# Kernel tuning notes

Hardware: AMD Instinct MI355X
Metric: run time of the kernel (lower is better)

Reference implementation:

```python
import jax, jax.numpy as jnp
import numpy as np

N_NODES = 100000
N_EDGES = 1600000
N_DATE = 5000  # last N_DATE nodes are date nodes [0,0,1]
D_IN = 128
D_H = 128
N_CLASSES = 16
MLP_HID = 8


def setup_inputs() -> dict:
    key = jax.random.key(0)
    ks = jax.random.split(key, 12)
    feature = jax.random.normal(ks[0], (N_NODES, D_IN), dtype=jnp.float32)
    edge_weight = jax.random.uniform(ks[1], (N_EDGES,), dtype=jnp.float32)
    src = jax.random.randint(ks[2], (N_EDGES,), 0, N_NODES, dtype=jnp.int32)
    dst = jax.random.randint(ks[3], (N_EDGES,), 0, N_NODES, dtype=jnp.int32)
    # node_type one-hot: regular nodes [1,0,0], last N_DATE nodes are date nodes [0,0,1]
    nt = np.zeros((N_NODES, 3), dtype=np.int32)
    nt[: N_NODES - N_DATE, 0] = 1
    nt[N_NODES - N_DATE :, 2] = 1
    node_type = jnp.asarray(nt)
    # GraphConv weights (xavier uniform) + zero bias, DGL convention: h @ W, W:[in,out]
    def xavier(k, fan_in, fan_out):
        lim = float(np.sqrt(6.0 / (fan_in + fan_out)))
        return jax.random.uniform(k, (fan_in, fan_out), jnp.float32, -lim, lim)
    W0 = xavier(ks[4], D_IN, D_H)
    b0 = jnp.zeros((D_H,), jnp.float32)
    W1 = xavier(ks[5], D_H, D_H)
    b1 = jnp.zeros((D_H,), jnp.float32)
    mlp_w1 = xavier(ks[6], D_H, MLP_HID)
    mlp_b1 = jnp.zeros((MLP_HID,), jnp.float32)
    mlp_w2 = xavier(ks[7], MLP_HID, N_CLASSES)
    mlp_b2 = jnp.zeros((N_CLASSES,), jnp.float32)
    return {
        "feature": feature, "edge_weight": edge_weight, "src": src, "dst": dst,
        "node_type": node_type, "W0": W0, "b0": b0, "W1": W1, "b1": b1,
        "mlp_w1": mlp_w1, "mlp_b1": mlp_b1, "mlp_w2": mlp_w2, "mlp_b2": mlp_b2,
    }


def reference(feature, edge_weight, src, dst, node_type,
              W0, b0, W1, b1, mlp_w1, mlp_b1, mlp_w2, mlp_b2):
    n = feature.shape[0]
    ones_e = jnp.ones_like(edge_weight)
    # unweighted degrees (DGL norm='both'), clamped to >= 1
    deg_out = jnp.clip(jax.ops.segment_sum(ones_e, src, num_segments=n), 1.0)
    deg_in = jnp.clip(jax.ops.segment_sum(ones_e, dst, num_segments=n), 1.0)
    norm_src = deg_out ** -0.5  # [N]
    norm_dst = deg_in ** -0.5   # [N]

    def graph_conv(h, W, b):
        hn = h * norm_src[:, None]                      # D_out^{-1/2} src scaling
        msg = hn[src] * edge_weight[:, None]            # [E, d] edge-weighted gather
        agg = jax.ops.segment_sum(msg, dst, num_segments=n)  # scatter-add
        return (agg * norm_dst[:, None]) @ W + b        # D_in^{-1/2}, then linear

    h = jax.nn.relu(graph_conv(feature, W0, b0))
    h = jax.nn.relu(graph_conv(h, W1, b1))

    # sum-pool over date nodes ([0,0,1]) == tail slice in original layout
    date_mask = ((node_type[:, 0] == 0) & (node_type[:, 1] == 0) & (node_type[:, 2] == 1)).astype(h.dtype)
    cnt = date_mask.sum()
    pooled = (h * date_mask[:, None]).sum(axis=0) / cnt  # [d_h]

    hid = jax.nn.relu(pooled @ mlp_w1 + mlp_b1)
    return hid @ mlp_w2 + mlp_b2  # [num_classes]
```

## Files before the change

### kernel.cpp

```cpp
#include <hip/hip_runtime.h>
#include <hip/hip_fp16.h>
#include <stdint.h>

#define D 128
#define GT 16
#define SLOTS 48
#define EPB 4096
#define PTB 1024
#define CAPE 5120
#define MAXB 400
#define MAXDATE 8192
#define WPN 16384

typedef _Float16 f16x8 __attribute__((ext_vector_type(8)));
typedef float    f32x4 __attribute__((ext_vector_type(4)));

__global__ __launch_bounds__(PTB) void partition_kernel(
    const int* __restrict__ src, const int* __restrict__ dst, const float* __restrict__ ew,
    int* __restrict__ cursorA, int* __restrict__ cursorB,
    int2* __restrict__ ebuf, int* __restrict__ sbuf, int E, int nbk) {
    __shared__ int histA[MAXB], histB[MAXB], baseA[MAXB], baseB[MAXB];
    int tid = threadIdx.x;
    for (int i = tid; i < nbk; i += PTB) { histA[i] = 0; histB[i] = 0; }
    __syncthreads();
    int e0 = blockIdx.x * EPB;
    int dcache[EPB / PTB], scache[EPB / PTB];
    float wcache[EPB / PTB];
    #pragma unroll
    for (int i = 0; i < EPB / PTB; ++i) {
        int e = e0 + i * PTB + tid;
        bool ok = e < E;
        dcache[i] = ok ? dst[e] : -1;
        scache[i] = ok ? src[e] : 0;
        wcache[i] = ok ? ew[e] : 0.f;
        if (ok) {
            atomicAdd(&histA[dcache[i] >> 8], 1);
            atomicAdd(&histB[scache[i] >> 8], 1);
        }
    }
    __syncthreads();
    for (int i = tid; i < nbk; i += PTB) {
        baseA[i] = atomicAdd(&cursorA[i], histA[i]);
        baseB[i] = atomicAdd(&cursorB[i], histB[i]);
        histA[i] = 0; histB[i] = 0;
    }
    __syncthreads();
    #pragma unroll
    for (int i = 0; i < EPB / PTB; ++i) {
        if (dcache[i] >= 0) {
            int d = dcache[i], s = scache[i];
            int bA = d >> 8;
            int pA = baseA[bA] + atomicAdd(&histA[bA], 1);
            if (pA < CAPE) ebuf[(size_t)bA * CAPE + pA] =
                make_int2(s | ((d & 255) << 17), __float_as_int(wcache[i]));
            int bB = s >> 8;
            int pB = baseB[bB] + atomicAdd(&histB[bB], 1);
            if (pB < CAPE) sbuf[(size_t)bB * CAPE + pB] = s;
        }
    }
}

__global__ __launch_bounds__(256) void build_count_kernel(
    const int2* __restrict__ ebuf, const int* __restrict__ cursorA,
    const int* __restrict__ sbuf, const int* __restrict__ cursorB,
    int2* __restrict__ ell, int* __restrict__ deg_in, int* __restrict__ deg_out,
    int n, int nbk) {
    __shared__ int lcur[256];
    int tid = threadIdx.x;
    lcur[tid] = 0;
    __syncthreads();
    if (blockIdx.x < (unsigned)nbk) {
        int b = blockIdx.x;
        int cntE = min(cursorA[b], CAPE);
        const int2* buf = ebuf + (size_t)b * CAPE;
        for (int i = tid; i < cntE; i += 256) {
            int2 r = buf[i];
            int s = r.x & 0x1FFFF;
            int dlow = (r.x >> 17) & 255;
            int slot = atomicAdd(&lcur[dlow], 1);
            int node = (b << 8) + dlow;
            if (slot < SLOTS) ell[(size_t)node * SLOTS + slot] = make_int2(s, r.y);
        }
        __syncthreads();
        int v = (b << 8) + tid;
        if (v < n) deg_in[v] = lcur[tid];
    } else {
        int b = blockIdx.x - nbk;
        int cntS = min(cursorB[b], CAPE);
        const int* buf = sbuf + (size_t)b * CAPE;
        for (int i = tid; i < cntS; i += 256) {
            atomicAdd(&lcur[buf[i] & 255], 1);
        }
        __syncthreads();
        int v = (b << 8) + tid;
        if (v < n) deg_out[v] = lcur[tid];
    }
}

__global__ void norm_flag_kernel(const int* __restrict__ deg_out, const int* __restrict__ deg_in,
                                 const int* __restrict__ node_type,
                                 float* __restrict__ norm_src, float* __restrict__ norm_dst,
                                 int* __restrict__ list, int* __restrict__ cnt, int n) {
    int v = blockIdx.x * blockDim.x + threadIdx.x;
    if (v < n) {
        float d_o = (float)max(deg_out[v], 1);
        float d_i = (float)max(deg_in[v], 1);
        norm_src[v] = 1.0f / sqrtf(d_o);
        norm_dst[v] = 1.0f / sqrtf(d_i);
        int t0 = node_type[v * 3 + 0];
        int t1 = node_type[v * 3 + 1];
        int t2 = node_type[v * 3 + 2];
        if (t0 == 0 && t1 == 0 && t2 == 1) {
            int idx = atomicAdd(cnt, 1);
            list[idx] = v;
        }
    }
}

__global__ __launch_bounds__(256) void wpack_kernel(const float* __restrict__ W,
                                                    _Float16* __restrict__ wp) {
    int base = blockIdx.x * 256 + threadIdx.x;
    for (int idx = base; idx < WPN; idx += gridDim.x * 256) {
        int j = idx & 7;
        int l = (idx >> 3) & 63;
        int c = (idx >> 9) & 7;
        int k0b = idx >> 12;
        int q = l >> 4, r = l & 15;
        float w = W[(k0b * 32 + q * 8 + j) * 128 + c * 16 + r];
        _Float16 hi = (_Float16)w;
        wp[idx] = hi;
        wp[idx + WPN] = (_Float16)(w - (float)hi);
    }
}

__global__ __launch_bounds__(256) void gemm_mfma_kernel(
    const float* __restrict__ X, const float* __restrict__ ns,
    const _Float16* __restrict__ wp, _Float16* __restrict__ P, int n) {
    int lane = threadIdx.x & 63;
    int wib  = threadIdx.x >> 6;
    int q = lane >> 4, r = lane & 15;
    int row0 = blockIdx.x * 128 + wib * 32;
    if (row0 >= n) return;
    int ra = min(row0 + r,      n - 1);
    int rb = min(row0 + 16 + r, n - 1);
    float sa = ns[ra];
    float sb = ns[rb];

    f32x4 acc[2][8];
    #pragma unroll
    for (int t = 0; t < 2; ++t)
        #pragma unroll
        for (int c = 0; c < 8; ++c)
            acc[t][c] = (f32x4){0.f, 0.f, 0.f, 0.f};

    for (int k0 = 0; k0 < 128; k0 += 32) {
        float4 xa0 = *(const float4*)&X[(size_t)ra * 128 + k0 + q * 8];
        float4 xa1 = *(const float4*)&X[(size_t)ra * 128 + k0 + q * 8 + 4];
        float4 xb0 = *(const float4*)&X[(size_t)rb * 128 + k0 + q * 8];
        float4 xb1 = *(const float4*)&X[(size_t)rb * 128 + k0 + q * 8 + 4];
        f16x8 a0, a1;
        a0[0] = (_Float16)(xa0.x * sa); a0[1] = (_Float16)(xa0.y * sa);
        a0[2] = (_Float16)(xa0.z * sa); a0[3] = (_Float16)(xa0.w * sa);
        a0[4] = (_Float16)(xa1.x * sa); a0[5] = (_Float16)(xa1.y * sa);
        a0[6] = (_Float16)(xa1.z * sa); a0[7] = (_Float16)(xa1.w * sa);
        a1[0] = (_Float16)(xb0.x * sb); a1[1] = (_Float16)(xb0.y * sb);
        a1[2] = (_Float16)(xb0.z * sb); a1[3] = (_Float16)(xb0.w * sb);
        a1[4] = (_Float16)(xb1.x * sb); a1[5] = (_Float16)(xb1.y * sb);
        a1[6] = (_Float16)(xb1.z * sb); a1[7] = (_Float16)(xb1.w * sb);
        const _Float16* wb = wp + (size_t)(k0 >> 5) * 4096 + lane * 8;
        #pragma unroll
        for (int c = 0; c < 8; ++c) {
            f16x8 bh = *(const f16x8*)&wb[c * 512];
            f16x8 bl = *(const f16x8*)&wb[c * 512 + WPN];
            acc[0][c] = __builtin_amdgcn_mfma_f32_16x16x32_f16(a0, bh, acc[0][c], 0, 0, 0);
            acc[0][c] = __builtin_amdgcn_mfma_f32_16x16x32_f16(a0, bl, acc[0][c], 0, 0, 0);
            acc[1][c] = __builtin_amdgcn_mfma_f32_16x16x32_f16(a1, bh, acc[1][c], 0, 0, 0);
            acc[1][c] = __builtin_amdgcn_mfma_f32_16x16x32_f16(a1, bl, acc[1][c], 0, 0, 0);
        }
    }

    #pragma unroll
    for (int t = 0; t < 2; ++t) {
        #pragma unroll
        for (int j = 0; j < 4; ++j) {
            int row = row0 + t * 16 + q * 4 + j;
            if (row < n) {
                #pragma unroll
                for (int c = 0; c < 8; ++c) {
                    P[(size_t)row * 128 + c * 16 + r] = (_Float16)acc[t][c][j];
                }
            }
        }
    }
}

__global__ __launch_bounds__(256) void gather1_kernel(
    const __half* __restrict__ P, const int* __restrict__ deg_in,
    const int2* __restrict__ ell, const float* __restrict__ norm_src,
    const float* __restrict__ norm_dst, const float* __restrict__ bias,
    __half* __restrict__ h1, int n) {
    int wave = (blockIdx.x * 256 + threadIdx.x) >> 6;
    int lane = threadIdx.x & 63;
    if (wave >= n) return;
    int v = __builtin_amdgcn_readfirstlane(wave);
    int m = min(deg_in[v], SLOTS);
    const int2* row = ell + (size_t)v * SLOTS;
    int half = lane >> 5;
    int l32  = lane & 31;
    float4 acc = make_float4(0.f, 0.f, 0.f, 0.f);
    for (int e = 0; e < m; e += 4) {
        int4 qa = *(const int4*)&row[e];
        int4 qb = *(const int4*)&row[e + 2];
        int2 p0 = half ? make_int2(qa.z, qa.w) : make_int2(qa.x, qa.y);
        int2 p1 = half ? make_int2(qb.z, qb.w) : make_int2(qb.x, qb.y);
        bool v0 = (e + half) < m;
        bool v1 = (e + 2 + half) < m;
        int s0 = v0 ? p0.x : 0;
        int s1 = v1 ? p1.x : 0;
        float2 raw0 = ((const float2*)P)[(size_t)s0 * 32 + l32];
        float2 raw1 = ((const float2*)P)[(size_t)s1 * 32 + l32];
        float w0 = v0 ? __int_as_float(p0.y) : 0.f;
        float w1 = v1 ? __int_as_float(p1.y) : 0.f;
        float2 a01 = __half22float2(*(const __half2*)&raw0.x);
        float2 a23 = __half22float2(*(const __half2*)&raw0.y);
        float2 b01 = __half22float2(*(const __half2*)&raw1.x);
        float2 b23 = __half22float2(*(const __half2*)&raw1.y);
        acc.x = fmaf(w0, a01.x, acc.x); acc.x = fmaf(w1, b01.x, acc.x);
        acc.y = fmaf(w0, a01.y, acc.y); acc.y = fmaf(w1, b01.y, acc.y);
        acc.z = fmaf(w0, a23.x, acc.z); acc.z = fmaf(w1, b23.x, acc.z);
        acc.w = fmaf(w0, a23.y, acc.w); acc.w = fmaf(w1, b23.y, acc.w);
    }
    acc.x += __shfl_xor(acc.x, 32);
    acc.y += __shfl_xor(acc.y, 32);
    acc.z += __shfl_xor(acc.z, 32);
    acc.w += __shfl_xor(acc.w, 32);
    if (half == 0) {
        float nd = norm_dst[v];
        float ns = norm_src[v];
        float4 b4 = ((const float4*)bias)[l32];
        float ra = fmaxf(fmaf(acc.x, nd, b4.x), 0.f) * ns;
        float rb = fmaxf(fmaf(acc.y, nd, b4.y), 0.f) * ns;
        float rc = fmaxf(fmaf(acc.z, nd, b4.z), 0.f) * ns;
        float rd = fmaxf(fmaf(acc.w, nd, b4.w), 0.f) * ns;
        __half2 h0 = __floats2half2_rn(ra, rb);
        __half2 h1v = __floats2half2_rn(rc, rd);
        uint2 u;
        u.x = *(unsigned int*)&h0;
        u.y = *(unsigned int*)&h1v;
        ((uint2*)h1)[(size_t)v * 32 + l32] = u;
    }
}

__global__ __launch_bounds__(256) void gather2_list_kernel(
    const __half* __restrict__ h, const int* __restrict__ deg_in,
    const int2* __restrict__ ell, const float* __restrict__ norm_dst,
    const int* __restrict__ list, const int* __restrict__ cnt,
    float* __restrict__ out) {
    int wave = (blockIdx.x * 256 + threadIdx.x) >> 6;
    int lane = threadIdx.x & 63;
    if (wave >= min(*cnt, MAXDATE)) return;
    int v = __builtin_amdgcn_readfirstlane(list[wave]);
    int m = min(deg_in[v], SLOTS);
    const int2* row = ell + (size_t)v * SLOTS;
    int half = lane >> 5;
    int l32  = lane & 31;
    float4 acc = make_float4(0.f, 0.f, 0.f, 0.f);
    for (int e = 0; e < m; e += 4) {
        int4 qa = *(const int4*)&row[e];
        int4 qb = *(const int4*)&row[e + 2];
        int2 p0 = half ? make_int2(qa.z, qa.w) : make_int2(qa.x, qa.y);
        int2 p1 = half ? make_int2(qb.z, qb.w) : make_int2(qb.x, qb.y);
        bool v0 = (e + half) < m;
        bool v1 = (e + 2 + half) < m;
        int s0 = v0 ? p0.x : 0;
        int s1 = v1 ? p1.x : 0;
        float2 raw0 = ((const float2*)h)[(size_t)s0 * 32 + l32];
        float2 raw1 = ((const float2*)h)[(size_t)s1 * 32 + l32];
        float w0 = v0 ? __int_as_float(p0.y) : 0.f;
        float w1 = v1 ? __int_as_float(p1.y) : 0.f;
        float2 a01 = __half22float2(*(const __half2*)&raw0.x);
        float2 a23 = __half22float2(*(const __half2*)&raw0.y);
        float2 b01 = __half22float2(*(const __half2*)&raw1.x);
        float2 b23 = __half22float2(*(const __half2*)&raw1.y);
        acc.x = fmaf(w0, a01.x, acc.x); acc.x = fmaf(w1, b01.x, acc.x);
        acc.y = fmaf(w0, a01.y, acc.y); acc.y = fmaf(w1, b01.y, acc.y);
        acc.z = fmaf(w0, a23.x, acc.z); acc.z = fmaf(w1, b23.x, acc.z);
        acc.w = fmaf(w0, a23.y, acc.w); acc.w = fmaf(w1, b23.y, acc.w);
    }
    acc.x += __shfl_xor(acc.x, 32);
    acc.y += __shfl_xor(acc.y, 32);
    acc.z += __shfl_xor(acc.z, 32);
    acc.w += __shfl_xor(acc.w, 32);
    if (half == 0) {
        float nd = norm_dst[v];
        ((float4*)(out + (size_t)wave * D))[l32] =
            make_float4(acc.x * nd, acc.y * nd, acc.z * nd, acc.w * nd);
    }
}

__global__ __launch_bounds__(256) void gemm_pool_kernel(
    const float* __restrict__ X, const float* __restrict__ W,
    const float* __restrict__ bias, const int* __restrict__ cnt,
    float* __restrict__ pooled) {
    __shared__ float rows[4][GT * D];
    int lane = threadIdx.x & 63;
    int wib  = threadIdx.x >> 6;
    int tile = blockIdx.x * 4 + wib;
    int t0 = tile * GT;
    int m = min(*cnt, MAXDATE);
    if (t0 >= m) return;

    float* rw = rows[wib];
    const float2* X2 = (const float2*)X;
    #pragma unroll
    for (int t = 0; t < GT; ++t) {
        int i = t0 + t;
        float2 r = (i < m) ? X2[(size_t)i * 64 + lane] : make_float2(0.f, 0.f);
        *(float2*)&rw[t * D + 2 * lane] = r;
    }
    __builtin_amdgcn_wave_barrier();

    float2 bb = ((const float2*)bias)[lane];
    float2 acc[GT];
    #pragma unroll
    for (int t = 0; t < GT; ++t) acc[t] = make_float2(0.f, 0.f);

    const float2* W2 = (const float2*)W;
    for (int k = 0; k < D; k += 4) {
        float2 w0 = W2[(k + 0) * 64 + lane];
        float2 w1 = W2[(k + 1) * 64 + lane];
        float2 w2 = W2[(k + 2) * 64 + lane];
        float2 w3 = W2[(k + 3) * 64 + lane];
        #pragma unroll
        for (int t = 0; t < GT; ++t) {
            float4 r = *(const float4*)&rw[t * D + k];
            acc[t].x = fmaf(r.x, w0.x, acc[t].x); acc[t].y = fmaf(r.x, w0.y, acc[t].y);
            acc[t].x = fmaf(r.y, w1.x, acc[t].x); acc[t].y = fmaf(r.y, w1.y, acc[t].y);
            acc[t].x = fmaf(r.z, w2.x, acc[t].x); acc[t].y = fmaf(r.z, w2.y, acc[t].y);
            acc[t].x = fmaf(r.w, w3.x, acc[t].x); acc[t].y = fmaf(r.w, w3.y, acc[t].y);
        }
    }

    float psx = 0.f, psy = 0.f;
    #pragma unroll
    for (int t = 0; t < GT; ++t) {
        if (t0 + t < m) {
            psx += fmaxf(acc[t].x + bb.x, 0.f);
            psy += fmaxf(acc[t].y + bb.y, 0.f);
        }
    }
    atomicAdd(&pooled[2 * lane + 0], psx);
    atomicAdd(&pooled[2 * lane + 1], psy);
}

__global__ void mlp_kernel(const float* __restrict__ pooled, const int* __restrict__ cnt,
                           const float* __restrict__ w1, const float* __restrict__ b1,
                           const float* __restrict__ w2, const float* __restrict__ b2,
                           float* __restrict__ out) {
    __shared__ float hid[8];
    int t = threadIdx.x;
    float inv = 1.0f / (float)(*cnt);
    if (t < 8) {
        float a = b1[t];
        for (int k = 0; k < 128; ++k) a = fmaf(pooled[k] * inv, w1[k * 8 + t], a);
        hid[t] = fmaxf(a, 0.f);
    }
    __syncthreads();
    if (t < 16) {
        float a = b2[t];
        for (int j = 0; j < 8; ++j) a = fmaf(hid[j], w2[j * 16 + t], a);
        out[t] = a;
    }
}

extern "C" void kernel_launch(void* const* d_in, const int* in_sizes, int n_in,
                              void* d_out, int out_size, void* d_ws, size_t ws_size,
                              hipStream_t stream) {
    const float* feature   = (const float*)d_in[0];
    const float* ew        = (const float*)d_in[1];
    const int*   src       = (const int*)d_in[2];
    const int*   dst       = (const int*)d_in[3];
    const int*   node_type = (const int*)d_in[4];
    const float* W0        = (const float*)d_in[5];
    const float* b0        = (const float*)d_in[6];
    const float* W1        = (const float*)d_in[7];
    const float* b1        = (const float*)d_in[8];
    const float* mw1       = (const float*)d_in[9];
    const float* mb1       = (const float*)d_in[10];
    const float* mw2       = (const float*)d_in[11];
    const float* mb2       = (const float*)d_in[12];
    float* out = (float*)d_out;

    const int n = in_sizes[0] / D;
    const int E = in_sizes[1];
    const int NBK = (n + 255) >> 8;

    char* ws = (char*)d_ws;
    size_t off = 0;
    auto alloc = [&](size_t bytes) -> void* {
        void* p = ws + off;
        off = (off + bytes + 255) & ~(size_t)255;
        return p;
    };
    int*      cursorAB = (int*)alloc(2 * MAXB * 4);
    int*      deg_in   = (int*)alloc((size_t)n * 4);
    int*      deg_out  = (int*)alloc((size_t)n * 4);
    float*    norm_src = (float*)alloc((size_t)n * 4);
    float*    norm_dst = (float*)alloc((size_t)n * 4);
    int*      list     = (int*)alloc((size_t)n * 4);
    int2*     ell      = (int2*)alloc(((size_t)n * SLOTS + 8) * 8);
    int2*     ebuf     = (int2*)alloc((size_t)NBK * CAPE * 8);
    int*      sbuf     = (int*)alloc((size_t)NBK * CAPE * 4);
    _Float16* P16      = (_Float16*)alloc((size_t)n * D * 2);
    __half*   h1       = (__half*)alloc((size_t)n * D * 2);
    _Float16* wp       = (_Float16*)alloc(2 * WPN * 2);
    float*    pooled   = (float*)alloc(D * 4);
    int*      cnt      = (int*)alloc(256);
    float*    agg      = (float*)sbuf;

    int* cursorA = cursorAB;
    int* cursorB = cursorAB + MAXB;

    hipMemsetAsync(cursorAB, 0, 2 * MAXB * 4, stream);
    hipMemsetAsync(pooled,   0, D * 4 + 256, stream);

    const int TB = 256;
    int pblk = (E + EPB - 1) / EPB;
    int nblk = (n + TB - 1) / TB;

    wpack_kernel<<<16, TB, 0, stream>>>(W0, wp);
    partition_kernel<<<pblk, PTB, 0, stream>>>(src, dst, ew, cursorA, cursorB, ebuf, sbuf, E, NBK);
    build_count_kernel<<<2 * NBK, TB, 0, stream>>>(ebuf, cursorA, sbuf, cursorB,
                                                   ell, deg_in, deg_out, n, NBK);
    norm_flag_kernel<<<nblk, TB, 0, stream>>>(deg_out, deg_in, node_type,
                                              norm_src, norm_dst, list, cnt, n);

    gemm_mfma_kernel<<<(n + 127) / 128, TB, 0, stream>>>(feature, norm_src, wp, P16, n);

    gather1_kernel<<<(n * 64 + TB - 1) / TB, TB, 0, stream>>>(
        (const __half*)P16, deg_in, ell, norm_src, norm_dst, b0, h1, n);

    gather2_list_kernel<<<(MAXDATE * 64) / TB, TB, 0, stream>>>(
        h1, deg_in, ell, norm_dst, list, cnt, agg);
    gemm_pool_kernel<<<((MAXDATE + GT - 1) / GT + 3) / 4, TB, 0, stream>>>(agg, W1, b1, cnt, pooled);

    mlp_kernel<<<1, 64, 0, stream>>>(pooled, cnt, mw1, mb1, mw2, mb2, out);
}
```

Baseline: 328.6 us.

## Store layer-1 projection in FP8 and fold memsets into weight pack kernel

The layer-1 GEMM output is quantized to FP8 e4m3 instead of fp16, and the edge gather reads 4 bytes per lane and decodes each byte to float. This halves the bytes fetched per gathered neighbor row in the dominant gather kernel. Buffer zeroing for cursors, pooled sums and the date counter moves into the weight-packing kernel, removing two memset launches. FP8 storage reduces precision of the intermediate, risking tolerance failures, and the scalar byte decoding adds ALU work.

```diff
diff --git a/kernel.cpp b/kernel.cpp
--- a/kernel.cpp
+++ b/kernel.cpp
@@ -1,5 +1,6 @@
 #include <hip/hip_runtime.h>
 #include <hip/hip_fp16.h>
+#include <hip/hip_fp8.h>
 #include <stdint.h>
 
 #define D 128
@@ -14,6 +15,12 @@
 
 typedef _Float16 f16x8 __attribute__((ext_vector_type(8)));
 typedef float    f32x4 __attribute__((ext_vector_type(4)));
+
+__device__ __forceinline__ float fp8_dec(unsigned char b) {
+    __hip_fp8_e4m3 t;
+    t.__x = b;
+    return (float)t;
+}
 
 __global__ __launch_bounds__(PTB) void partition_kernel(
     const int* __restrict__ src, const int* __restrict__ dst, const float* __restrict__ ew,
@@ -118,8 +125,17 @@
 }
 
 __global__ __launch_bounds__(256) void wpack_kernel(const float* __restrict__ W,
-                                                    _Float16* __restrict__ wp) {
-    int base = blockIdx.x * 256 + threadIdx.x;
+                                                    _Float16* __restrict__ wp,
+                                                    int* __restrict__ cursorAB,
+                                                    float* __restrict__ pooled,
+                                                    int* __restrict__ cnt) {
+    int tid = threadIdx.x;
+    if (blockIdx.x == 0) {
+        for (int i = tid; i < 2 * MAXB; i += 256) cursorAB[i] = 0;
+        if (tid < D) pooled[tid] = 0.f;
+        if (tid == 0) *cnt = 0;
+    }
+    int base = blockIdx.x * 256 + tid;
     for (int idx = base; idx < WPN; idx += gridDim.x * 256) {
         int j = idx & 7;
         int l = (idx >> 3) & 63;
@@ -135,7 +151,7 @@
 
 __global__ __launch_bounds__(256) void gemm_mfma_kernel(
     const float* __restrict__ X, const float* __restrict__ ns,
-    const _Float16* __restrict__ wp, _Float16* __restrict__ P, int n) {
+    const _Float16* __restrict__ wp, unsigned char* __restrict__ P8, int n) {
     int lane = threadIdx.x & 63;
     int wib  = threadIdx.x >> 6;
     int q = lane >> 4, r = lane & 15;
@@ -187,7 +203,8 @@
             if (row < n) {
                 #pragma unroll
                 for (int c = 0; c < 8; ++c) {
-                    P[(size_t)row * 128 + c * 16 + r] = (_Float16)acc[t][c][j];
+                    __hip_fp8_e4m3 qv((float)acc[t][c][j]);
+                    P8[(size_t)row * 128 + c * 16 + r] = qv.__x;
                 }
             }
         }
@@ -195,7 +212,7 @@
 }
 
 __global__ __launch_bounds__(256) void gather1_kernel(
-    const __half* __restrict__ P, const int* __restrict__ deg_in,
+    const unsigned char* __restrict__ P8, const int* __restrict__ deg_in,
     const int2* __restrict__ ell, const float* __restrict__ norm_src,
     const float* __restrict__ norm_dst, const float* __restrict__ bias,
     __half* __restrict__ h1, int n) {
@@ -207,6 +224,7 @@
     const int2* row = ell + (size_t)v * SLOTS;
     int half = lane >> 5;
     int l32  = lane & 31;
+    const unsigned int* P32 = (const unsigned int*)P8;
     float4 acc = make_float4(0.f, 0.f, 0.f, 0.f);
     for (int e = 0; e < m; e += 4) {
         int4 qa = *(const int4*)&row[e];
@@ -217,18 +235,19 @@
         bool v1 = (e + 2 + half) < m;
         int s0 = v0 ? p0.x : 0;
         int s1 = v1 ? p1.x : 0;
-        float2 raw0 = ((const float2*)P)[(size_t)s0 * 32 + l32];
-        float2 raw1 = ((const float2*)P)[(size_t)s1 * 32 + l32];
-        float w0 = v0 ? __int_as_float(p0.y) : 0.f;
+        unsigned int r0 = P32[(size_t)s0 * 32 + l32];
+        unsigned int r1 = P32[(size_t)s1 * 32 + l32];
+        float w0 = v0 ? __int_as_float(p0.y) * __builtin_amdgcn_readfirstlane(0x3f800000 ? 1.f : 1.f) : 0.f;
+        w0 = v0 ? __int_as_float(p0.y) : 0.f;
         float w1 = v1 ? __int_as_float(p1.y) : 0.f;
-        float2 a01 = __half22float2(*(const __half2*)&raw0.x);
-        float2 a23 = __half22float2(*(const __half2*)&raw0.y);
-        float2 b01 = __half22float2(*(const __half2*)&raw1.x);
-        float2 b23 = __half22float2(*(const __half2*)&raw1.y);
-        acc.x = fmaf(w0, a01.x, acc.x); acc.x = fmaf(w1, b01.x, acc.x);
-        acc.y = fmaf(w0, a01.y, acc.y); acc.y = fmaf(w1, b01.y, acc.y);
-        acc.z = fmaf(w0, a23.x, acc.z); acc.z = fmaf(w1, b23.x, acc.z);
-        acc.w = fmaf(w0, a23.y, acc.w); acc.w = fmaf(w1, b23.y, acc.w);
+        acc.x = fmaf(w0, fp8_dec(r0 & 0xff),         acc.x);
+        acc.y = fmaf(w0, fp8_dec((r0 >> 8) & 0xff),  acc.y);
+        acc.z = fmaf(w0, fp8_dec((r0 >> 16) & 0xff), acc.z);
+        acc.w = fmaf(w0, fp8_dec(r0 >> 24),          acc.w);
+        acc.x = fmaf(w1, fp8_dec(r1 & 0xff),         acc.x);
+        acc.y = fmaf(w1, fp8_dec((r1 >> 8) & 0xff),  acc.y);
+        acc.z = fmaf(w1, fp8_dec((r1 >> 16) & 0xff), acc.z);
+        acc.w = fmaf(w1, fp8_dec(r1 >> 24),          acc.w);
     }
     acc.x += __shfl_xor(acc.x, 32);
     acc.y += __shfl_xor(acc.y, 32);
@@ -402,43 +421,40 @@
         off = (off + bytes + 255) & ~(size_t)255;
         return p;
     };
-    int*      cursorAB = (int*)alloc(2 * MAXB * 4);
-    int*      deg_in   = (int*)alloc((size_t)n * 4);
-    int*      deg_out  = (int*)alloc((size_t)n * 4);
-    float*    norm_src = (float*)alloc((size_t)n * 4);
-    float*    norm_dst = (float*)alloc((size_t)n * 4);
-    int*      list     = (int*)alloc((size_t)n * 4);
-    int2*     ell      = (int2*)alloc(((size_t)n * SLOTS + 8) * 8);
-    int2*     ebuf     = (int2*)alloc((size_t)NBK * CAPE * 8);
-    int*      sbuf     = (int*)alloc((size_t)NBK * CAPE * 4);
-    _Float16* P16      = (_Float16*)alloc((size_t)n * D * 2);
-    __half*   h1       = (__half*)alloc((size_t)n * D * 2);
-    _Float16* wp       = (_Float16*)alloc(2 * WPN * 2);
-    float*    pooled   = (float*)alloc(D * 4);
-    int*      cnt      = (int*)alloc(256);
-    float*    agg      = (float*)sbuf;
+    int*           cursorAB = (int*)alloc(2 * MAXB * 4);
+    int*           deg_in   = (int*)alloc((size_t)n * 4);
+    int*           deg_out  = (int*)alloc((size_t)n * 4);
+    float*         norm_src = (float*)alloc((size_t)n * 4);
+    float*         norm_dst = (float*)alloc((size_t)n * 4);
+    int*           list     = (int*)alloc((size_t)n * 4);
+    int2*          ell      = (int2*)alloc(((size_t)n * SLOTS + 8) * 8);
+    int2*          ebuf     = (int2*)alloc((size_t)NBK * CAPE * 8);
+    int*           sbuf     = (int*)alloc((size_t)NBK * CAPE * 4);
+    unsigned char* P8       = (unsigned char*)alloc((size_t)n * D);
+    __half*        h1       = (__half*)alloc((size_t)n * D * 2);
+    _Float16*      wp       = (_Float16*)alloc(2 * WPN * 2);
+    float*         pooled   = (float*)alloc(D * 4);
+    int*           cnt      = (int*)alloc(256);
+    float*         agg      = (float*)sbuf;
 
     int* cursorA = cursorAB;
     int* cursorB = cursorAB + MAXB;
-
-    hipMemsetAsync(cursorAB, 0, 2 * MAXB * 4, stream);
-    hipMemsetAsync(pooled,   0, D * 4 + 256, stream);
 
     const int TB = 256;
     int pblk = (E + EPB - 1) / EPB;
     int nblk = (n + TB - 1) / TB;
 
-    wpack_kernel<<<16, TB, 0, stream>>>(W0, wp);
+    wpack_kernel<<<16, TB, 0, stream>>>(W0, wp, cursorAB, pooled, cnt);
     partition_kernel<<<pblk, PTB, 0, stream>>>(src, dst, ew, cursorA, cursorB, ebuf, sbuf, E, NBK);
     build_count_kernel<<<2 * NBK, TB, 0, stream>>>(ebuf, cursorA, sbuf, cursorB,
                                                    ell, deg_in, deg_out, n, NBK);
     norm_flag_kernel<<<nblk, TB, 0, stream>>>(deg_out, deg_in, node_type,
                                               norm_src, norm_dst, list, cnt, n);
 
-    gemm_mfma_kernel<<<(n + 127) / 128, TB, 0, stream>>>(feature, norm_src, wp, P16, n);
+    gemm_mfma_kernel<<<(n + 127) / 128, TB, 0, stream>>>(feature, norm_src, wp, P8, n);
 
     gather1_kernel<<<(n * 64 + TB - 1) / TB, TB, 0, stream>>>(
-        (const __half*)P16, deg_in, ell, norm_src, norm_dst, b0, h1, n);
+        P8, deg_in, ell, norm_src, norm_dst, b0, h1, n);
 
     gather2_list_kernel<<<(MAXDATE * 64) / TB, TB, 0, stream>>>(
         h1, deg_in, ell, norm_dst, list, cnt, agg);
```

New measurement: 313.7 us. -4.5%, faster.
